# Kernel optimization log

Measured on AMD Instinct MI355X. Metric: run time of the kernel, lower is better.

The kernel has to match this reference:

```python
import jax, jax.numpy as jnp
import numpy as np

DEGREE = 4  # sh degree -> DEGREE**2 = 16 components
RES = 128
N_PTS = 2097152
CH = 3


def sh_components(degree, d):
    """Real SH basis values for unit directions d [..., 3] -> [..., degree**2]."""
    x, y, z = d[..., 0], d[..., 1], d[..., 2]
    xx, yy, zz = x * x, y * y, z * z
    xy, yz, xz = x * y, y * z, x * z
    comps = [jnp.full(x.shape, 0.28209479177387814, dtype=d.dtype)]
    if degree > 1:
        comps += [-0.4886025119029199 * y,
                  0.4886025119029199 * z,
                  -0.4886025119029199 * x]
    if degree > 2:
        comps += [1.0925484305920792 * xy,
                  -1.0925484305920792 * yz,
                  0.31539156525252005 * (2.0 * zz - xx - yy),
                  -1.0925484305920792 * xz,
                  0.5462742152960396 * (xx - yy)]
    if degree > 3:
        comps += [-0.5900435899266435 * y * (3 * xx - yy),
                  2.890611442640554 * xy * z,
                  -0.4570457994644658 * y * (4 * zz - xx - yy),
                  0.3731763325901154 * z * (2 * zz - 3 * xx - 3 * yy),
                  -0.4570457994644658 * x * (4 * zz - xx - yy),
                  1.445305721320277 * z * (xx - yy),
                  -0.5900435899266435 * x * (xx - 3 * yy)]
    if degree > 4:
        comps += [2.5033429417967046 * xy * (xx - yy),
                  -1.7701307697799304 * yz * (3 * xx - yy),
                  0.9461746957575601 * xy * (7 * zz - 1),
                  -0.6690465435572892 * yz * (7 * zz - 3),
                  0.10578554691520431 * (zz * (35 * zz - 30) + 3),
                  -0.6690465435572892 * xz * (7 * zz - 3),
                  0.47308734787878004 * (xx - yy) * (7 * zz - 1),
                  -1.7701307697799304 * xz * (xx - 3 * yy),
                  0.6258357354491761 * (xx * (xx - 3 * yy) - yy * (3 * xx - yy))]
    return jnp.stack(comps, axis=-1)


def trilerp(coefficients, aabb, points):
    """Trilinear interpolation of grid coefficients [R,R,R,D2,C] at points [N,3] -> [N,D2,C]."""
    res = coefficients.shape[0]
    amin, amax = aabb[:3], aabb[3:]
    g = (points - amin) / (amax - amin) * (res - 1)       # continuous grid coords
    g = jnp.clip(g, 0.0, res - 1.0)
    i0 = jnp.clip(jnp.floor(g).astype(jnp.int32), 0, res - 2)  # [N,3]
    f = g - i0.astype(g.dtype)                            # fractional part [N,3]
    fx, fy, fz = f[..., 0], f[..., 1], f[..., 2]
    out = None
    for dx in (0, 1):
        wx = fx if dx else (1.0 - fx)
        for dy in (0, 1):
            wy = fy if dy else (1.0 - fy)
            for dz in (0, 1):
                wz = fz if dz else (1.0 - fz)
                w = (wx * wy * wz)[:, None, None]          # [N,1,1]
                c = coefficients[i0[:, 0] + dx, i0[:, 1] + dy, i0[:, 2] + dz]  # [N,D2,C]
                out = w * c if out is None else out + w * c
    return out


def setup_inputs() -> dict:
    key = jax.random.key(0)
    k1, k2, k3 = jax.random.split(key, 3)
    coefficients = jax.random.normal(k1, (RES, RES, RES, DEGREE ** 2, CH), dtype=jnp.float32) * 0.1
    aabb = jnp.array([-1.0, -1.0, -1.0, 1.0, 1.0, 1.0], dtype=jnp.float32)
    points = jax.random.uniform(k2, (N_PTS, 3), dtype=jnp.float32) * 2.0 - 1.0  # inside aabb
    normals = jax.random.normal(k3, (N_PTS, 3), dtype=jnp.float32)
    normals = normals / jnp.linalg.norm(normals, axis=-1, keepdims=True)
    return {"coefficients": coefficients, "aabb": aabb, "points": points, "normals": normals}


def reference(coefficients, aabb, points, normals):
    comps = sh_components(DEGREE, normals)                 # [N, D2]
    ic = trilerp(coefficients, aabb, points)               # [N, D2, C]
    irradiance = jnp.sum(ic * comps[..., None], axis=1)    # [N, C]
    return jnp.maximum(irradiance, 0.0)
```

## Files before the change

kernel.cpp:

```cpp
#include <hip/hip_runtime.h>


constexpr int RES = 128;
constexpr int D2 = 16;
constexpr int CSTRIDE = D2 * 3;
constexpr int CELL_F4 = CSTRIDE / 4;

constexpr int NBX = 32, NBY = 16, NBZ = 16;
constexpr int NBINS = NBX * NBY * NBZ;
constexpr int HX = 5, HY = 9, HZ = 9;
constexpr int TOT_F4 = HX * HY * HZ * CELL_F4;
constexpr int MAIN_THREADS = 256;
constexpr int LOAD_ITERS = (TOT_F4 + MAIN_THREADS - 1) / MAIN_THREADS;

constexpr int REPL = 4;
constexpr int CAP = 104;
constexpr int CNT_PAD = 16;
constexpr int OVF_CAP = 131072;

__device__ __forceinline__ void grid_coords(const float* aabb, float px, float py, float pz,
                                            int& ix, int& iy, int& iz,
                                            float& fx, float& fy, float& fz)
{
    const float a0 = aabb[0], a1 = aabb[1], a2 = aabb[2];
    const float b0 = aabb[3], b1 = aabb[4], b2 = aabb[5];
    float gx = (px - a0) / (b0 - a0) * (float)(RES - 1);
    float gy = (py - a1) / (b1 - a1) * (float)(RES - 1);
    float gz = (pz - a2) / (b2 - a2) * (float)(RES - 1);
    gx = fminf(fmaxf(gx, 0.0f), (float)(RES - 1));
    gy = fminf(fmaxf(gy, 0.0f), (float)(RES - 1));
    gz = fminf(fmaxf(gz, 0.0f), (float)(RES - 1));
    ix = min((int)floorf(gx), RES - 2);
    iy = min((int)floorf(gy), RES - 2);
    iz = min((int)floorf(gz), RES - 2);
    fx = gx - (float)ix;
    fy = gy - (float)iy;
    fz = gz - (float)iz;
}

__device__ __forceinline__ int bin_of(int ix, int iy, int iz)
{
    return (((ix >> 2) * NBY) + (iy >> 3)) * NBZ + (iz >> 3);
}

__device__ __forceinline__ void sh_basis(float nx, float ny, float nz, float* sh)
{
    const float xx = nx * nx, yy = ny * ny, zz = nz * nz;
    const float xy = nx * ny, yz = ny * nz, xz = nx * nz;
    sh[0]  = 0.28209479177387814f;
    sh[1]  = -0.4886025119029199f * ny;
    sh[2]  = 0.4886025119029199f * nz;
    sh[3]  = -0.4886025119029199f * nx;
    sh[4]  = 1.0925484305920792f * xy;
    sh[5]  = -1.0925484305920792f * yz;
    sh[6]  = 0.31539156525252005f * (2.0f * zz - xx - yy);
    sh[7]  = -1.0925484305920792f * xz;
    sh[8]  = 0.5462742152960396f * (xx - yy);
    sh[9]  = -0.5900435899266435f * ny * (3.0f * xx - yy);
    sh[10] = 2.890611442640554f * xy * nz;
    sh[11] = -0.4570457994644658f * ny * (4.0f * zz - xx - yy);
    sh[12] = 0.3731763325901154f * nz * (2.0f * zz - 3.0f * xx - 3.0f * yy);
    sh[13] = -0.4570457994644658f * nx * (4.0f * zz - xx - yy);
    sh[14] = 1.445305721320277f * nz * (xx - yy);
    sh[15] = -0.5900435899266435f * nx * (xx - 3.0f * yy);
}

__device__ void compute_point_global(
    const float* __restrict__ coeff,
    const float* __restrict__ aabb,
    const float* __restrict__ points,
    const float* __restrict__ normals,
    float* __restrict__ out, int i)
{
    const float px = points[3 * i + 0], py = points[3 * i + 1], pz = points[3 * i + 2];
    const float nx = normals[3 * i + 0], ny = normals[3 * i + 1], nz = normals[3 * i + 2];
    int ix, iy, iz; float fx, fy, fz;
    grid_coords(aabb, px, py, pz, ix, iy, iz, fx, fy, fz);
    float sh[D2];
    sh_basis(nx, ny, nz, sh);
    const float wz0 = 1.0f - fz, wz1 = fz;
    float acc0 = 0.0f, acc1 = 0.0f, acc2 = 0.0f;
#pragma unroll
    for (int dx = 0; dx < 2; ++dx) {
        const float wx = dx ? fx : 1.0f - fx;
#pragma unroll
        for (int dy = 0; dy < 2; ++dy) {
            const float wxy = wx * (dy ? fy : 1.0f - fy);
            const int cell = (((ix + dx) * RES + (iy + dy)) * RES + iz) * CSTRIDE;
            const float4* __restrict__ cp = (const float4*)(coeff + cell);
            union { float4 q[24]; float v[96]; } u;
#pragma unroll
            for (int kk = 0; kk < 24; ++kk) u.q[kk] = cp[kk];
            float s00 = 0.f, s01 = 0.f, s02 = 0.f;
            float s10 = 0.f, s11 = 0.f, s12 = 0.f;
#pragma unroll
            for (int j = 0; j < D2; ++j) {
                const float s = sh[j];
                s00 = fmaf(s, u.v[3 * j + 0], s00);
                s01 = fmaf(s, u.v[3 * j + 1], s01);
                s02 = fmaf(s, u.v[3 * j + 2], s02);
                s10 = fmaf(s, u.v[48 + 3 * j + 0], s10);
                s11 = fmaf(s, u.v[48 + 3 * j + 1], s11);
                s12 = fmaf(s, u.v[48 + 3 * j + 2], s12);
            }
            const float w0 = wxy * wz0, w1 = wxy * wz1;
            acc0 = fmaf(w0, s00, fmaf(w1, s10, acc0));
            acc1 = fmaf(w0, s01, fmaf(w1, s11, acc1));
            acc2 = fmaf(w0, s02, fmaf(w1, s12, acc2));
        }
    }
    out[3 * i + 0] = fmaxf(acc0, 0.0f);
    out[3 * i + 1] = fmaxf(acc1, 0.0f);
    out[3 * i + 2] = fmaxf(acc2, 0.0f);
}

__global__ __launch_bounds__(256) void scatter_kernel(
    const float* __restrict__ aabb,
    const float* __restrict__ points,
    int* __restrict__ cnt_p,
    int* __restrict__ slots,
    int* __restrict__ ovf_cnt,
    int* __restrict__ ovf,
    int n)
{
    const int i = blockIdx.x * blockDim.x + threadIdx.x;
    if (i >= n) return;
    int ix, iy, iz; float fx, fy, fz;
    grid_coords(aabb, points[3 * i + 0], points[3 * i + 1], points[3 * i + 2],
                ix, iy, iz, fx, fy, fz);
    const int bin = bin_of(ix, iy, iz);
    const int rep = (i >> 6) & (REPL - 1);
    const int g = bin * REPL + rep;
    const int pos = atomicAdd(&cnt_p[g * CNT_PAD], 1);
    if (pos < CAP) {
        slots[g * CAP + pos] = i;
    } else {
        const int o = atomicAdd(&ovf_cnt[0], 1);
        if (o < OVF_CAP) ovf[o] = i;
        else ovf_cnt[1] = 1;
    }
}

__global__ __launch_bounds__(MAIN_THREADS) void main_kernel(
    const float* __restrict__ coeff,
    const float* __restrict__ aabb,
    const float* __restrict__ points,
    const float* __restrict__ normals,
    const int* __restrict__ cnt_p,
    const int* __restrict__ slots,
    float* __restrict__ out)
{
    extern __shared__ char smem[];
    float4* lds4 = (float4*)smem;

    const int bin = blockIdx.x;
    const int c0 = min(cnt_p[(bin * REPL + 0) * CNT_PAD], CAP);
    const int c1 = min(cnt_p[(bin * REPL + 1) * CNT_PAD], CAP);
    const int c2 = min(cnt_p[(bin * REPL + 2) * CNT_PAD], CAP);
    const int c3 = min(cnt_p[(bin * REPL + 3) * CNT_PAD], CAP);
    const int tot = c0 + c1 + c2 + c3;
    if (tot == 0) return;

    const int bx = bin / (NBY * NBZ);
    const int by = (bin / NBZ) % NBY;
    const int bz = bin % NBZ;
    const int x0 = bx << 2;
    const int y0 = by << 3;
    const int z0 = bz << 3;

    const int tid = threadIdx.x;
    const float4* __restrict__ coeff4 = (const float4*)coeff;

#pragma unroll
    for (int k = 0; k < LOAD_ITERS; ++k) {
        const int u = tid + k * MAIN_THREADS;
        if (u < TOT_F4) {
            int cx = u / (HY * HZ * CELL_F4);
            int r1 = u - cx * (HY * HZ * CELL_F4);
            int cy = r1 / (HZ * CELL_F4);
            int r2 = r1 - cy * (HZ * CELL_F4);
            int cz = r2 / CELL_F4;
            int kk = r2 - cz * CELL_F4;
            int xg = min(x0 + cx, RES - 1);
            int yg = min(y0 + cy, RES - 1);
            int zg = min(z0 + cz, RES - 1);
            lds4[u] = coeff4[((xg * RES + yg) * RES + zg) * CELL_F4 + kk];
        }
    }
    __syncthreads();

    for (int t = tid; t < tot; t += MAIN_THREADS) {
        int k = t, r = 0;
        if (k >= c0) { k -= c0; r = 1;
            if (k >= c1) { k -= c1; r = 2;
                if (k >= c2) { k -= c2; r = 3; } } }
        const int i = slots[(bin * REPL + r) * CAP + k];

        const float px = points[3 * i + 0];
        const float py = points[3 * i + 1];
        const float pz = points[3 * i + 2];
        const float nx = normals[3 * i + 0];
        const float ny = normals[3 * i + 1];
        const float nz = normals[3 * i + 2];

        int ix, iy, iz; float fx, fy, fz;
        grid_coords(aabb, px, py, pz, ix, iy, iz, fx, fy, fz);
        const int lx = ix - x0, ly = iy - y0, lz = iz - z0;

        float sh[D2];
        sh_basis(nx, ny, nz, sh);

        const float wz0 = 1.0f - fz, wz1 = fz;
        float acc0 = 0.0f, acc1 = 0.0f, acc2 = 0.0f;

#pragma unroll
        for (int dx = 0; dx < 2; ++dx) {
            const float wx = dx ? fx : 1.0f - fx;
#pragma unroll
            for (int dy = 0; dy < 2; ++dy) {
                const float wxy = wx * (dy ? fy : 1.0f - fy);
                const int lcell = (((lx + dx) * HY + (ly + dy)) * HZ + lz) * CELL_F4;
                union { float4 q[24]; float v[96]; } u;
#pragma unroll
                for (int kk = 0; kk < 24; ++kk) u.q[kk] = lds4[lcell + kk];

                float s00 = 0.f, s01 = 0.f, s02 = 0.f;
                float s10 = 0.f, s11 = 0.f, s12 = 0.f;
#pragma unroll
                for (int j = 0; j < D2; ++j) {
                    const float s = sh[j];
                    s00 = fmaf(s, u.v[3 * j + 0], s00);
                    s01 = fmaf(s, u.v[3 * j + 1], s01);
                    s02 = fmaf(s, u.v[3 * j + 2], s02);
                    s10 = fmaf(s, u.v[48 + 3 * j + 0], s10);
                    s11 = fmaf(s, u.v[48 + 3 * j + 1], s11);
                    s12 = fmaf(s, u.v[48 + 3 * j + 2], s12);
                }
                const float w0 = wxy * wz0, w1 = wxy * wz1;
                acc0 = fmaf(w0, s00, fmaf(w1, s10, acc0));
                acc1 = fmaf(w0, s01, fmaf(w1, s11, acc1));
                acc2 = fmaf(w0, s02, fmaf(w1, s12, acc2));
            }
        }

        out[3 * i + 0] = fmaxf(acc0, 0.0f);
        out[3 * i + 1] = fmaxf(acc1, 0.0f);
        out[3 * i + 2] = fmaxf(acc2, 0.0f);
    }
}

__global__ __launch_bounds__(256) void overflow_kernel(
    const float* __restrict__ coeff,
    const float* __restrict__ aabb,
    const float* __restrict__ points,
    const float* __restrict__ normals,
    const int* __restrict__ ovf_cnt,
    const int* __restrict__ ovf,
    const int* __restrict__ cnt_p,
    const int* __restrict__ slots,
    float* __restrict__ out,
    int n)
{
    const int m = min(ovf_cnt[0], OVF_CAP);
    for (int t = blockIdx.x * blockDim.x + threadIdx.x; t < m; t += gridDim.x * blockDim.x)
        compute_point_global(coeff, aabb, points, normals, out, ovf[t]);

    if (ovf_cnt[1]) {
        for (int i = blockIdx.x * blockDim.x + threadIdx.x; i < n; i += gridDim.x * blockDim.x) {
            int ix, iy, iz; float fx, fy, fz;
            grid_coords(aabb, points[3 * i + 0], points[3 * i + 1], points[3 * i + 2],
                        ix, iy, iz, fx, fy, fz);
            const int g = bin_of(ix, iy, iz) * REPL + ((i >> 6) & (REPL - 1));
            const int c = min(cnt_p[g * CNT_PAD], CAP);
            bool placed = false;
            for (int k = 0; k < c && !placed; ++k) placed = (slots[g * CAP + k] == i);
            for (int k = 0; k < m && !placed; ++k)  placed = (ovf[k] == i);
            if (!placed) compute_point_global(coeff, aabb, points, normals, out, i);
        }
    }
}

__global__ __launch_bounds__(256) void direct_kernel(
    const float* __restrict__ coeff,
    const float* __restrict__ aabb,
    const float* __restrict__ points,
    const float* __restrict__ normals,
    float* __restrict__ out,
    int n)
{
    const int i = blockIdx.x * blockDim.x + threadIdx.x;
    if (i >= n) return;
    compute_point_global(coeff, aabb, points, normals, out, i);
}

extern "C" void kernel_launch(void* const* d_in, const int* in_sizes, int n_in,
                              void* d_out, int out_size, void* d_ws, size_t ws_size,
                              hipStream_t stream) {
    const float* coeff   = (const float*)d_in[0];
    const float* aabb    = (const float*)d_in[1];
    const float* points  = (const float*)d_in[2];
    const float* normals = (const float*)d_in[3];
    float* out = (float*)d_out;

    const int n = in_sizes[2] / 3;
    const int nblk = (n + 255) / 256;

    size_t off = 0;
    auto take = [&](size_t bytes) { size_t o = off; off = (off + bytes + 255) & ~(size_t)255; return o; };
    char* ws = (char*)d_ws;
    const size_t cnt_bytes = (size_t)NBINS * REPL * CNT_PAD * 4;
    const size_t o_cnt   = take(cnt_bytes);
    const size_t o_ovfc  = take(256);
    const size_t o_slots = take((size_t)NBINS * REPL * CAP * 4);
    const size_t o_ovf   = take((size_t)OVF_CAP * 4);
    const size_t needed = off;

    if (ws_size < needed) {
        hipLaunchKernelGGL(direct_kernel, dim3(nblk), dim3(256), 0, stream,
                           coeff, aabb, points, normals, out, n);
        return;
    }

    int* cnt_p   = (int*)(ws + o_cnt);
    int* ovf_cnt = (int*)(ws + o_ovfc);
    int* slots   = (int*)(ws + o_slots);
    int* ovf     = (int*)(ws + o_ovf);

    hipMemsetAsync(ws + o_cnt, 0, cnt_bytes + 256, stream);

    hipLaunchKernelGGL(scatter_kernel, dim3(nblk), dim3(256), 0, stream,
                       aabb, points, cnt_p, slots, ovf_cnt, ovf, n);
    hipLaunchKernelGGL(main_kernel, dim3(NBINS), dim3(MAIN_THREADS),
                       TOT_F4 * sizeof(float4), stream,
                       coeff, aabb, points, normals, cnt_p, slots, out);
    hipLaunchKernelGGL(overflow_kernel, dim3(64), dim3(256), 0, stream,
                       coeff, aabb, points, normals, ovf_cnt, ovf, cnt_p, slots, out, n);
}
```

Measured before the change: 828.3 us.

## Pad LDS coefficient columns and fold overflow handling into main kernel

The shared-memory tile now stores each (x,y) column of cells with one extra float4 of padding. This shifts bank alignment between columns to reduce LDS bank conflicts during the per-point 24-float4 reads. The separate overflow kernel launch is removed, and block 0 of the main kernel handles overflow points after its own bin. This saves a launch and a dependency, but all overflow work now runs on a single 256-thread block instead of 64 blocks, which could create a long tail if many points overflow.

```diff
diff --git a/kernel.cpp b/kernel.cpp
--- a/kernel.cpp
+++ b/kernel.cpp
@@ -9,9 +9,14 @@
 constexpr int NBX = 32, NBY = 16, NBZ = 16;
 constexpr int NBINS = NBX * NBY * NBZ;
 constexpr int HX = 5, HY = 9, HZ = 9;
-constexpr int TOT_F4 = HX * HY * HZ * CELL_F4;
 constexpr int MAIN_THREADS = 256;
-constexpr int LOAD_ITERS = (TOT_F4 + MAIN_THREADS - 1) / MAIN_THREADS;
+
+constexpr int SRC_COL_F4 = HZ * CELL_F4;
+constexpr int COL_F4 = SRC_COL_F4 + 1;
+constexpr int NCOL = HX * HY;
+constexpr int TOT_SRC_F4 = NCOL * SRC_COL_F4;
+constexpr int LDS_F4 = NCOL * COL_F4;
+constexpr int LOAD_ITERS = (TOT_SRC_F4 + MAIN_THREADS - 1) / MAIN_THREADS;
 
 constexpr int REPL = 4;
 constexpr int CAP = 104;
@@ -148,134 +153,130 @@
     const float* __restrict__ normals,
     const int* __restrict__ cnt_p,
     const int* __restrict__ slots,
-    float* __restrict__ out)
+    const int* __restrict__ ovf_cnt,
+    const int* __restrict__ ovf,
+    float* __restrict__ out,
+    int n)
 {
     extern __shared__ char smem[];
     float4* lds4 = (float4*)smem;
 
     const int bin = blockIdx.x;
+    const int tid = threadIdx.x;
+    const bool ovf_block = (bin == 0);
+
     const int c0 = min(cnt_p[(bin * REPL + 0) * CNT_PAD], CAP);
     const int c1 = min(cnt_p[(bin * REPL + 1) * CNT_PAD], CAP);
     const int c2 = min(cnt_p[(bin * REPL + 2) * CNT_PAD], CAP);
     const int c3 = min(cnt_p[(bin * REPL + 3) * CNT_PAD], CAP);
     const int tot = c0 + c1 + c2 + c3;
-    if (tot == 0) return;
-
-    const int bx = bin / (NBY * NBZ);
-    const int by = (bin / NBZ) % NBY;
-    const int bz = bin % NBZ;
-    const int x0 = bx << 2;
-    const int y0 = by << 3;
-    const int z0 = bz << 3;
-
-    const int tid = threadIdx.x;
-    const float4* __restrict__ coeff4 = (const float4*)coeff;
-
-#pragma unroll
-    for (int k = 0; k < LOAD_ITERS; ++k) {
-        const int u = tid + k * MAIN_THREADS;
-        if (u < TOT_F4) {
-            int cx = u / (HY * HZ * CELL_F4);
-            int r1 = u - cx * (HY * HZ * CELL_F4);
-            int cy = r1 / (HZ * CELL_F4);
-            int r2 = r1 - cy * (HZ * CELL_F4);
-            int cz = r2 / CELL_F4;
-            int kk = r2 - cz * CELL_F4;
-            int xg = min(x0 + cx, RES - 1);
-            int yg = min(y0 + cy, RES - 1);
-            int zg = min(z0 + cz, RES - 1);
-            lds4[u] = coeff4[((xg * RES + yg) * RES + zg) * CELL_F4 + kk];
-        }
-    }
-    __syncthreads();
-
-    for (int t = tid; t < tot; t += MAIN_THREADS) {
-        int k = t, r = 0;
-        if (k >= c0) { k -= c0; r = 1;
-            if (k >= c1) { k -= c1; r = 2;
-                if (k >= c2) { k -= c2; r = 3; } } }
-        const int i = slots[(bin * REPL + r) * CAP + k];
-
-        const float px = points[3 * i + 0];
-        const float py = points[3 * i + 1];
-        const float pz = points[3 * i + 2];
-        const float nx = normals[3 * i + 0];
-        const float ny = normals[3 * i + 1];
-        const float nz = normals[3 * i + 2];
-
-        int ix, iy, iz; float fx, fy, fz;
-        grid_coords(aabb, px, py, pz, ix, iy, iz, fx, fy, fz);
-        const int lx = ix - x0, ly = iy - y0, lz = iz - z0;
-
-        float sh[D2];
-        sh_basis(nx, ny, nz, sh);
-
-        const float wz0 = 1.0f - fz, wz1 = fz;
-        float acc0 = 0.0f, acc1 = 0.0f, acc2 = 0.0f;
-
-#pragma unroll
-        for (int dx = 0; dx < 2; ++dx) {
-            const float wx = dx ? fx : 1.0f - fx;
-#pragma unroll
-            for (int dy = 0; dy < 2; ++dy) {
-                const float wxy = wx * (dy ? fy : 1.0f - fy);
-                const int lcell = (((lx + dx) * HY + (ly + dy)) * HZ + lz) * CELL_F4;
-                union { float4 q[24]; float v[96]; } u;
-#pragma unroll
-                for (int kk = 0; kk < 24; ++kk) u.q[kk] = lds4[lcell + kk];
-
-                float s00 = 0.f, s01 = 0.f, s02 = 0.f;
-                float s10 = 0.f, s11 = 0.f, s12 = 0.f;
-#pragma unroll
-                for (int j = 0; j < D2; ++j) {
-                    const float s = sh[j];
-                    s00 = fmaf(s, u.v[3 * j + 0], s00);
-                    s01 = fmaf(s, u.v[3 * j + 1], s01);
-                    s02 = fmaf(s, u.v[3 * j + 2], s02);
-                    s10 = fmaf(s, u.v[48 + 3 * j + 0], s10);
-                    s11 = fmaf(s, u.v[48 + 3 * j + 1], s11);
-                    s12 = fmaf(s, u.v[48 + 3 * j + 2], s12);
-                }
-                const float w0 = wxy * wz0, w1 = wxy * wz1;
-                acc0 = fmaf(w0, s00, fmaf(w1, s10, acc0));
-                acc1 = fmaf(w0, s01, fmaf(w1, s11, acc1));
-                acc2 = fmaf(w0, s02, fmaf(w1, s12, acc2));
+    if (tot == 0 && !ovf_block) return;
+
+    if (tot > 0) {
+        const int bx = bin / (NBY * NBZ);
+        const int by = (bin / NBZ) % NBY;
+        const int bz = bin % NBZ;
+        const int x0 = bx << 2;
+        const int y0 = by << 3;
+        const int z0 = bz << 3;
+
+        const float4* __restrict__ coeff4 = (const float4*)coeff;
+
+#pragma unroll
+        for (int k = 0; k < LOAD_ITERS; ++k) {
+            const int u = tid + k * MAIN_THREADS;
+            if (u < TOT_SRC_F4) {
+                int col = u / SRC_COL_F4;
+                int rem = u - col * SRC_COL_F4;
+                int cx = col / HY;
+                int cy = col - cx * HY;
+                int cz = rem / CELL_F4;
+                int kk = rem - cz * CELL_F4;
+                int xg = min(x0 + cx, RES - 1);
+                int yg = min(y0 + cy, RES - 1);
+                int zg = min(z0 + cz, RES - 1);
+                lds4[col * COL_F4 + rem] = coeff4[((xg * RES + yg) * RES + zg) * CELL_F4 + kk];
             }
         }
-
-        out[3 * i + 0] = fmaxf(acc0, 0.0f);
-        out[3 * i + 1] = fmaxf(acc1, 0.0f);
-        out[3 * i + 2] = fmaxf(acc2, 0.0f);
-    }
-}
-
-__global__ __launch_bounds__(256) void overflow_kernel(
-    const float* __restrict__ coeff,
-    const float* __restrict__ aabb,
-    const float* __restrict__ points,
-    const float* __restrict__ normals,
-    const int* __restrict__ ovf_cnt,
-    const int* __restrict__ ovf,
-    const int* __restrict__ cnt_p,
-    const int* __restrict__ slots,
-    float* __restrict__ out,
-    int n)
-{
-    const int m = min(ovf_cnt[0], OVF_CAP);
-    for (int t = blockIdx.x * blockDim.x + threadIdx.x; t < m; t += gridDim.x * blockDim.x)
-        compute_point_global(coeff, aabb, points, normals, out, ovf[t]);
-
-    if (ovf_cnt[1]) {
-        for (int i = blockIdx.x * blockDim.x + threadIdx.x; i < n; i += gridDim.x * blockDim.x) {
+        __syncthreads();
+
+        for (int t = tid; t < tot; t += MAIN_THREADS) {
+            int k = t, r = 0;
+            if (k >= c0) { k -= c0; r = 1;
+                if (k >= c1) { k -= c1; r = 2;
+                    if (k >= c2) { k -= c2; r = 3; } } }
+            const int i = slots[(bin * REPL + r) * CAP + k];
+
+            const float px = points[3 * i + 0];
+            const float py = points[3 * i + 1];
+            const float pz = points[3 * i + 2];
+            const float nx = normals[3 * i + 0];
+            const float ny = normals[3 * i + 1];
+            const float nz = normals[3 * i + 2];
+
             int ix, iy, iz; float fx, fy, fz;
-            grid_coords(aabb, points[3 * i + 0], points[3 * i + 1], points[3 * i + 2],
-                        ix, iy, iz, fx, fy, fz);
-            const int g = bin_of(ix, iy, iz) * REPL + ((i >> 6) & (REPL - 1));
-            const int c = min(cnt_p[g * CNT_PAD], CAP);
-            bool placed = false;
-            for (int k = 0; k < c && !placed; ++k) placed = (slots[g * CAP + k] == i);
-            for (int k = 0; k < m && !placed; ++k)  placed = (ovf[k] == i);
-            if (!placed) compute_point_global(coeff, aabb, points, normals, out, i);
+            grid_coords(aabb, px, py, pz, ix, iy, iz, fx, fy, fz);
+            const int lx = ix - x0, ly = iy - y0, lz = iz - z0;
+
+            float sh[D2];
+            sh_basis(nx, ny, nz, sh);
+
+            const float wz0 = 1.0f - fz, wz1 = fz;
+            float acc0 = 0.0f, acc1 = 0.0f, acc2 = 0.0f;
+
+#pragma unroll
+            for (int dx = 0; dx < 2; ++dx) {
+                const float wx = dx ? fx : 1.0f - fx;
+#pragma unroll
+                for (int dy = 0; dy < 2; ++dy) {
+                    const float wxy = wx * (dy ? fy : 1.0f - fy);
+                    const int lbase = ((lx + dx) * HY + (ly + dy)) * COL_F4 + lz * CELL_F4;
+                    union { float4 q[24]; float v[96]; } u;
+#pragma unroll
+                    for (int kk = 0; kk < 24; ++kk) u.q[kk] = lds4[lbase + kk];
+
+                    float s00 = 0.f, s01 = 0.f, s02 = 0.f;
+                    float s10 = 0.f, s11 = 0.f, s12 = 0.f;
+#pragma unroll
+                    for (int j = 0; j < D2; ++j) {
+                        const float s = sh[j];
+                        s00 = fmaf(s, u.v[3 * j + 0], s00);
+                        s01 = fmaf(s, u.v[3 * j + 1], s01);
+                        s02 = fmaf(s, u.v[3 * j + 2], s02);
+                        s10 = fmaf(s, u.v[48 + 3 * j + 0], s10);
+                        s11 = fmaf(s, u.v[48 + 3 * j + 1], s11);
+                        s12 = fmaf(s, u.v[48 + 3 * j + 2], s12);
+                    }
+                    const float w0 = wxy * wz0, w1 = wxy * wz1;
+                    acc0 = fmaf(w0, s00, fmaf(w1, s10, acc0));
+                    acc1 = fmaf(w0, s01, fmaf(w1, s11, acc1));
+                    acc2 = fmaf(w0, s02, fmaf(w1, s12, acc2));
+                }
+            }
+
+            out[3 * i + 0] = fmaxf(acc0, 0.0f);
+            out[3 * i + 1] = fmaxf(acc1, 0.0f);
+            out[3 * i + 2] = fmaxf(acc2, 0.0f);
+        }
+    }
+
+    if (ovf_block) {
+        const int m = min(ovf_cnt[0], OVF_CAP);
+        for (int t = tid; t < m; t += MAIN_THREADS)
+            compute_point_global(coeff, aabb, points, normals, out, ovf[t]);
+
+        if (ovf_cnt[1]) {
+            for (int i = tid; i < n; i += MAIN_THREADS) {
+                int ix, iy, iz; float fx, fy, fz;
+                grid_coords(aabb, points[3 * i + 0], points[3 * i + 1], points[3 * i + 2],
+                            ix, iy, iz, fx, fy, fz);
+                const int g = bin_of(ix, iy, iz) * REPL + ((i >> 6) & (REPL - 1));
+                const int c = min(cnt_p[g * CNT_PAD], CAP);
+                bool placed = false;
+                for (int k = 0; k < c && !placed; ++k) placed = (slots[g * CAP + k] == i);
+                for (int k = 0; k < m && !placed; ++k)  placed = (ovf[k] == i);
+                if (!placed) compute_point_global(coeff, aabb, points, normals, out, i);
+            }
         }
     }
 }
@@ -331,8 +332,6 @@
     hipLaunchKernelGGL(scatter_kernel, dim3(nblk), dim3(256), 0, stream,
                        aabb, points, cnt_p, slots, ovf_cnt, ovf, n);
     hipLaunchKernelGGL(main_kernel, dim3(NBINS), dim3(MAIN_THREADS),
-                       TOT_F4 * sizeof(float4), stream,
-                       coeff, aabb, points, normals, cnt_p, slots, out);
-    hipLaunchKernelGGL(overflow_kernel, dim3(64), dim3(256), 0, stream,
-                       coeff, aabb, points, normals, ovf_cnt, ovf, cnt_p, slots, out, n);
-}
+                       LDS_F4 * sizeof(float4), stream,
+                       coeff, aabb, points, normals, cnt_p, slots, ovf_cnt, ovf, out, n);
+}
```

After: 794.8 us. 1.04x faster.
